# Kernel tuning notes

Hardware: AMD Instinct MI355X
Metric: run time of the kernel (lower is better)

## Reference

```python
import jax, jax.numpy as jnp
import numpy as np
import math

D_MODEL = 1024
NUM_HEADS = 16
BATCH = 4
SEQ = 2048

def setup_inputs() -> dict:
    key = jax.random.key(0)
    ks = jax.random.split(key, 7)
    s = 1.0 / math.sqrt(D_MODEL)
    return {
        "x": jax.random.normal(ks[0], (BATCH, SEQ, D_MODEL), dtype=jnp.float32),
        "Wq": jax.random.normal(ks[1], (D_MODEL, D_MODEL), dtype=jnp.float32) * s,
        "bq": jax.random.normal(ks[2], (D_MODEL,), dtype=jnp.float32) * s,
        "Wk": jax.random.normal(ks[3], (D_MODEL, D_MODEL), dtype=jnp.float32) * s,
        "bk": jax.random.normal(ks[4], (D_MODEL,), dtype=jnp.float32) * s,
        "Wv": jax.random.normal(ks[5], (D_MODEL, D_MODEL), dtype=jnp.float32) * s,
        "bv": jax.random.normal(ks[6], (D_MODEL,), dtype=jnp.float32) * s,
        "num_heads": NUM_HEADS,
    }

def reference(x, Wq, bq, Wk, bk, Wv, bv, num_heads):
    B, S, D = x.shape
    hd = D // num_heads
    scale = 1.0 / math.sqrt(D)  # NOTE: module scales by sqrt(d_model), not sqrt(head_dim)
    # torch nn.Linear: y = x @ W.T + b
    q = x @ Wq.T + bq
    k = x @ Wk.T + bk
    v = x @ Wv.T + bv
    # Faithful replication of the module's (non-standard) row-major view:
    # (B, S, D) -> (B*H, S, D/H)
    q = q.reshape(B * num_heads, -1, hd)
    k = k.reshape(B * num_heads, -1, hd)
    v = v.reshape(B * num_heads, -1, hd)
    scores = jnp.einsum('bqd,bkd->bqk', q, k) * scale  # [B*H, S, S]
    probs = jax.nn.softmax(scores, axis=-1)
    out = jnp.einsum('bqk,bkd->bqd', probs, v)
    return out.reshape(B, -1, D)
```

## Files before the change

kernel.cpp:

```cpp
#include <hip/hip_runtime.h>
#include <stdint.h>

typedef unsigned short u16;
typedef __attribute__((ext_vector_type(8))) short short8;
typedef __attribute__((ext_vector_type(4))) float f32x4;
typedef __attribute__((ext_vector_type(16))) float f32x16;
typedef __attribute__((ext_vector_type(2))) unsigned int uv2;
typedef __attribute__((ext_vector_type(4))) unsigned int uv4;

#define MFMA16(a, b, c) __builtin_amdgcn_mfma_f32_16x16x32_bf16((a), (b), (c), 0, 0, 0)
#define MFMA32(a, b, c) __builtin_amdgcn_mfma_f32_32x32x16_bf16((a), (b), (c), 0, 0, 0)
#define LOG2E 1.4426950408889634f
#define SCALE 0.03125f
#define KC (SCALE * LOG2E)

__device__ __forceinline__ u16 f2bf(float f) {
  union { float f; uint32_t u; } cv; cv.f = f;
  uint32_t u = cv.u;
  uint32_t r = (u + 0x7fffu + ((u >> 16) & 1u)) >> 16;
  return (u16)r;
}

__device__ __forceinline__ unsigned cvtpk(float lo, float hi) {
  unsigned r;
  asm("v_cvt_pk_bf16_f32 %0, %1, %2" : "=v"(r) : "v"(lo), "v"(hi));
  return r;
}

__device__ __forceinline__ void gld(const void* g, void* l) {
  __builtin_amdgcn_global_load_lds(
      (const __attribute__((address_space(1))) void*)g,
      (__attribute__((address_space(3))) void*)l, 16, 0, 0);
}

__device__ __forceinline__ const short8* tile8(const u16* base, int row, int c) {
  return (const short8*)(base + row * 64 + (((c) ^ (row & 7)) << 3));
}

__global__ void cvt4_kernel(const float* __restrict__ x, const float* __restrict__ wq,
                            const float* __restrict__ wk, const float* __restrict__ wv,
                            u16* __restrict__ xb, u16* __restrict__ wqb,
                            u16* __restrict__ wkb, u16* __restrict__ wvb) {
  const int NX8 = 1048576;
  const int NW8 = 131072;
  const int TOT = NX8 + 3 * NW8;
  int i = blockIdx.x * blockDim.x + threadIdx.x;
  const int stride = gridDim.x * blockDim.x;
  for (; i < TOT; i += stride) {
    const float* src; u16* dst; int j;
    if (i < NX8) { src = x; dst = xb; j = i; }
    else if (i < NX8 + NW8) { src = wq; dst = wqb; j = i - NX8; }
    else if (i < NX8 + 2 * NW8) { src = wk; dst = wkb; j = i - NX8 - NW8; }
    else { src = wv; dst = wvb; j = i - NX8 - 2 * NW8; }
    const f32x4* s = (const f32x4*)src + (size_t)j * 2;
    f32x4 a = s[0], b = s[1];
    short8 o;
    o[0] = (short)f2bf(a[0]); o[1] = (short)f2bf(a[1]);
    o[2] = (short)f2bf(a[2]); o[3] = (short)f2bf(a[3]);
    o[4] = (short)f2bf(b[0]); o[5] = (short)f2bf(b[1]);
    o[6] = (short)f2bf(b[2]); o[7] = (short)f2bf(b[3]);
    *((short8*)dst + j) = o;
  }
}

__global__ __launch_bounds__(256) void gemm_qkv(
    const u16* __restrict__ xb,
    const u16* __restrict__ wqb, const u16* __restrict__ wkb, const u16* __restrict__ wvb,
    const float* __restrict__ bq, const float* __restrict__ bk, const float* __restrict__ bv,
    u16* __restrict__ qo, u16* __restrict__ ko, u16* __restrict__ vo) {
  __shared__ __align__(16) u16 sm[2][128 * 64];

  const int bid = blockIdx.x;
  const int cx = bid & 7, qq = bid >> 3;
  const int m = ((qq & 7) << 3) + cx;
  const int nz = qq >> 3;
  const int n = nz / 3;
  const int z = nz - n * 3;
  const u16* W = (z == 0) ? wqb : (z == 1) ? wkb : wvb;
  const float* bias = (z == 0) ? bq : (z == 1) ? bk : bv;
  u16* out = (z == 0) ? qo : (z == 1) ? ko : vo;
  const float oscale = (z == 0) ? KC : 1.0f;
  const int m0 = m * 128, n0 = n * 128;

  const int t = threadIdx.x;
  const int lane = t & 63;
  const int w = t >> 6;
  const int l15 = lane & 15, l4 = lane >> 4;
  const int mw = (w >> 1) * 64, nw = (w & 1) * 64;

  const int srow8 = lane >> 3;
  const int ssw = ((lane & 7) ^ srow8) << 3;
  const u16* aG = xb + (size_t)(m0 + (w * 4) * 8 + srow8) * 1024 + ssw;
  const u16* bG = W + (size_t)(n0 + (w * 4) * 8 + srow8) * 1024 + ssw;
  u16* aL = &sm[0][0] + (w * 4) * 512 + lane * 8;
  u16* bL = &sm[1][0] + (w * 4) * 512 + lane * 8;

  float biasv[4];
#pragma unroll
  for (int nj = 0; nj < 4; nj++) biasv[nj] = bias[n0 + nw + nj * 16 + l15];

  const f32x4 fz = {0.f, 0.f, 0.f, 0.f};
  f32x4 acc[4][4];
#pragma unroll
  for (int i = 0; i < 4; i++)
#pragma unroll
    for (int j = 0; j < 4; j++) acc[i][j] = fz;

  for (int k0 = 0; k0 < 1024; k0 += 64) {
    __syncthreads();
#pragma unroll
    for (int cc = 0; cc < 4; cc++) {
      gld(aG + k0 + (size_t)cc * 8 * 1024, aL + cc * 512);
      gld(bG + k0 + (size_t)cc * 8 * 1024, bL + cc * 512);
    }
    __syncthreads();
#pragma unroll
    for (int kk = 0; kk < 2; kk++) {
      short8 af[4], bf[4];
#pragma unroll
      for (int mi = 0; mi < 4; mi++) af[mi] = *tile8(&sm[0][0], mw + mi * 16 + l15, kk * 4 + l4);
#pragma unroll
      for (int nj = 0; nj < 4; nj++) bf[nj] = *tile8(&sm[1][0], nw + nj * 16 + l15, kk * 4 + l4);
      __builtin_amdgcn_s_setprio(1);
#pragma unroll
      for (int mi = 0; mi < 4; mi++)
#pragma unroll
        for (int nj = 0; nj < 4; nj++)
          acc[mi][nj] = MFMA16(af[mi], bf[nj], acc[mi][nj]);
      __builtin_amdgcn_s_setprio(0);
    }
  }

  __syncthreads();
  u16* Cs = &sm[0][0] + w * 4096;
#pragma unroll
  for (int mi = 0; mi < 4; mi++)
#pragma unroll
    for (int nj = 0; nj < 4; nj++)
#pragma unroll
      for (int r = 0; r < 4; r++) {
        const int row = mi * 16 + l4 * 4 + r;
        const int col = nj * 16 + l15;
        Cs[row * 64 + (((col >> 3) ^ (row & 7)) << 3) + (col & 7)] =
            f2bf((acc[mi][nj][r] + biasv[nj]) * oscale);
      }
#pragma unroll
  for (int i = 0; i < 8; i++) {
    const int row = i * 8 + (lane >> 3);
    short8 vv = *tile8(Cs, row, lane & 7);
    *(short8*)(out + (size_t)(m0 + mw + row) * 1024 + n0 + nw + (lane & 7) * 8) = vv;
  }
}

__global__ void repack_v(const u16* __restrict__ v, u16* __restrict__ vpk) {
  __shared__ u16 L[4096];
  const int g = blockIdx.y, tt = blockIdx.x;
  const u16* src = v + (size_t)g * 131072 + (size_t)tt * 4096;
  const int t = threadIdx.x;
#pragma unroll
  for (int i = 0; i < 2; i++) {
    const int ccc = t + i * 256;
    const int r = ccc >> 3, d0 = (ccc & 7) * 8;
    short8 d = *(const short8*)(src + r * 64 + d0);
    const int c = r >> 3, j = r & 7;
    const int h2 = d0 >> 5;
    const int base = h2 * 2048 + (c >> 1) * 512 + (c & 1) * 256 + j;
#pragma unroll
    for (int jj = 0; jj < 8; jj++) L[base + ((d0 & 31) + jj) * 8] = (u16)d[jj];
  }
  __syncthreads();
  u16* dst = vpk + (size_t)((size_t)g * 32 + tt) * 4096;
#pragma unroll
  for (int i = 0; i < 2; i++) {
    const int ccc = t + i * 256;
    *(short8*)(dst + ccc * 8) = *(const short8*)(L + ccc * 8);
  }
}


__device__ __forceinline__ void qblock(f32x16& s, float& lsum, f32x16& o0, f32x16& o1,
                                       const short8* vf) {
  float p[16];
  float ps = 0.f;
#pragma unroll
  for (int i = 0; i < 16; i++) {
    p[i] = __builtin_amdgcn_exp2f(s[i]);
    ps += p[i];
  }
  lsum += ps;

  short8 pa0, pa1;
  {
    unsigned a0 = cvtpk(p[0], p[1]);
    unsigned a1 = cvtpk(p[2], p[3]);
    unsigned b0 = cvtpk(p[4], p[5]);
    unsigned b1 = cvtpk(p[6], p[7]);
    uv2 r0 = __builtin_amdgcn_permlane32_swap(a0, b0, false, false);
    uv2 r1 = __builtin_amdgcn_permlane32_swap(a1, b1, false, false);
    union { uv4 u; short8 s8; } cc;
    cc.u[0] = r0[0]; cc.u[1] = r1[0]; cc.u[2] = r0[1]; cc.u[3] = r1[1];
    pa0 = cc.s8;
  }
  {
    unsigned a0 = cvtpk(p[8], p[9]);
    unsigned a1 = cvtpk(p[10], p[11]);
    unsigned b0 = cvtpk(p[12], p[13]);
    unsigned b1 = cvtpk(p[14], p[15]);
    uv2 r0 = __builtin_amdgcn_permlane32_swap(a0, b0, false, false);
    uv2 r1 = __builtin_amdgcn_permlane32_swap(a1, b1, false, false);
    union { uv4 u; short8 s8; } cc;
    cc.u[0] = r0[0]; cc.u[1] = r1[0]; cc.u[2] = r0[1]; cc.u[3] = r1[1];
    pa1 = cc.s8;
  }
  __builtin_amdgcn_s_setprio(1);
  o0 = MFMA32(pa0, vf[0], o0);
  o0 = MFMA32(pa1, vf[1], o0);
  o1 = MFMA32(pa0, vf[2], o1);
  o1 = MFMA32(pa1, vf[3], o1);
  __builtin_amdgcn_s_setprio(0);
}

__global__ __launch_bounds__(256, 4) void attn_kernel(const u16* __restrict__ q,
                                                      const u16* __restrict__ k,
                                                      const u16* __restrict__ vpk,
                                                      float* __restrict__ out) {
  __shared__ __align__(16) u16 Ks[2][64 * 64];
  const int t = threadIdx.x, lane = t & 63, w = t >> 6;
  const int l31 = lane & 31, hi = lane >> 5;
  const int bid = blockIdx.x;
  const int cx = bid & 7, qq = bid >> 3;
  const int qt = qq & 15;
  const int g = ((qq >> 4) << 3) + cx;
  const size_t gb = (size_t)g * 131072;
  const int q0 = qt * 128 + w * 32;

  const u16* qp = q + gb + (size_t)(q0 + l31) * 64 + hi * 8;
  short8 qf[4];
#pragma unroll
  for (int ks = 0; ks < 4; ks++) qf[ks] = *(const short8*)(qp + ks * 16);

  const int srow8 = lane >> 3;
  const int ssw = ((lane & 7) ^ srow8) << 3;
  const u16* kG = k + gb + (size_t)((w * 2) * 8 + srow8) * 64 + ssw;
  const u16* vB = vpk + (size_t)g * 131072 + (size_t)lane * 8;

  f32x16 o0, o1;
#pragma unroll
  for (int i = 0; i < 16; i++) { o0[i] = 0.f; o1[i] = 0.f; }
  float lsum = 0.f;

  {
    u16* kD = &Ks[0][0] + (w * 2) * 512 + lane * 8;
#pragma unroll
    for (int cc = 0; cc < 2; cc++) gld(kG + (size_t)cc * 8 * 64, kD + cc * 512);
  }
  __syncthreads();

  int cur = 0;
  for (int tt = 0; tt < 32; ++tt) {
    if (tt < 31) {
      const int kvn = (tt + 1) * 64;
      u16* kD = &Ks[cur ^ 1][0] + (w * 2) * 512 + lane * 8;
#pragma unroll
      for (int cc = 0; cc < 2; cc++)
        gld(kG + (size_t)kvn * 64 + (size_t)cc * 8 * 64, kD + cc * 512);
    }
    const u16* Kb = &Ks[cur][0];
    const u16* vT = vB + (size_t)tt * 4096;
#pragma unroll
    for (int b = 0; b < 2; b++) {
      short8 vf[4];
#pragma unroll
      for (int h2 = 0; h2 < 2; h2++)
#pragma unroll
        for (int ksp = 0; ksp < 2; ksp++)
          vf[h2 * 2 + ksp] = *(const short8*)(vT + h2 * 2048 + ((b << 1) | ksp) * 512);
      f32x16 s;
#pragma unroll
      for (int i = 0; i < 16; i++) s[i] = 0.f;
      __builtin_amdgcn_s_setprio(1);
#pragma unroll
      for (int ks = 0; ks < 4; ks++) {
        short8 kf = *tile8(Kb, b * 32 + l31, (ks << 1) | hi);
        s = MFMA32(kf, qf[ks], s);
      }
      __builtin_amdgcn_s_setprio(0);
      qblock(s, lsum, o0, o1, vf);
    }
    __syncthreads();
    cur ^= 1;
  }

  float lt = lsum + __shfl_xor(lsum, 32);
  float inv = 1.0f / lt;
  float* ob = out + gb + (size_t)q0 * 64;
#pragma unroll
  for (int r = 0; r < 16; r++) {
    int qr = (r & 3) + 8 * (r >> 2) + 4 * hi;
    float ir = __shfl(inv, qr);
    ob[(size_t)qr * 64 + l31] = o0[r] * ir;
    ob[(size_t)qr * 64 + 32 + l31] = o1[r] * ir;
  }
}

extern "C" void kernel_launch(void* const* d_in, const int* in_sizes, int n_in,
                              void* d_out, int out_size, void* d_ws, size_t ws_size,
                              hipStream_t stream) {
  const float* x  = (const float*)d_in[0];
  const float* Wq = (const float*)d_in[1];
  const float* bq = (const float*)d_in[2];
  const float* Wk = (const float*)d_in[3];
  const float* bk = (const float*)d_in[4];
  const float* Wv = (const float*)d_in[5];
  const float* bv = (const float*)d_in[6];
  float* out = (float*)d_out;

  const size_t NX = 8388608;
  const size_t NW = 1048576;
  u16* ws = (u16*)d_ws;
  u16* xb  = ws;
  u16* wqb = xb + NX;
  u16* wkb = wqb + NW;
  u16* wvb = wkb + NW;
  u16* qb  = wvb + NW;
  u16* kb  = qb + NX;
  u16* vb  = kb + NX;
  u16* vpk = vb + NX;

  cvt4_kernel<<<2048, 256, 0, stream>>>(x, Wq, Wk, Wv, xb, wqb, wkb, wvb);

  gemm_qkv<<<1536, 256, 0, stream>>>(xb, wqb, wkb, wvb, bq, bk, bv, qb, kb, vb);

  repack_v<<<dim3(32, 64), 256, 0, stream>>>(vb, vpk);

  attn_kernel<<<1024, 256, 0, stream>>>(qb, kb, vpk, out);
}
```

Measured before the change: 154.9 us.

## Pre-pack K into MFMA fragment layout and load K directly from global

```diff
diff --git a/kernel.cpp b/kernel.cpp
--- a/kernel.cpp
+++ b/kernel.cpp
@@ -152,28 +152,34 @@
   }
 }
 
-__global__ void repack_v(const u16* __restrict__ v, u16* __restrict__ vpk) {
-  __shared__ u16 L[4096];
+__global__ void repack_kv(const u16* __restrict__ k, const u16* __restrict__ v,
+                          u16* __restrict__ kpk, u16* __restrict__ vpk) {
+  __shared__ __align__(16) u16 LK[4096];
+  __shared__ u16 LV[4096];
   const int g = blockIdx.y, tt = blockIdx.x;
-  const u16* src = v + (size_t)g * 131072 + (size_t)tt * 4096;
+  const size_t sb = (size_t)g * 131072 + (size_t)tt * 4096;
   const int t = threadIdx.x;
 #pragma unroll
   for (int i = 0; i < 2; i++) {
     const int ccc = t + i * 256;
     const int r = ccc >> 3, d0 = (ccc & 7) * 8;
-    short8 d = *(const short8*)(src + r * 64 + d0);
+    short8 dk = *(const short8*)(k + sb + (size_t)r * 64 + d0);
+    const int b = r >> 5, ks = d0 >> 4;
+    const int L = (r & 31) | (((d0 >> 3) & 1) << 5);
+    *(short8*)(LK + ((b * 4 + ks) << 9) + L * 8) = dk;
+    short8 dv = *(const short8*)(v + sb + (size_t)r * 64 + d0);
     const int c = r >> 3, j = r & 7;
     const int h2 = d0 >> 5;
     const int base = h2 * 2048 + (c >> 1) * 512 + (c & 1) * 256 + j;
 #pragma unroll
-    for (int jj = 0; jj < 8; jj++) L[base + ((d0 & 31) + jj) * 8] = (u16)d[jj];
+    for (int jj = 0; jj < 8; jj++) LV[base + ((d0 & 31) + jj) * 8] = (u16)dv[jj];
   }
   __syncthreads();
-  u16* dst = vpk + (size_t)((size_t)g * 32 + tt) * 4096;
 #pragma unroll
   for (int i = 0; i < 2; i++) {
     const int ccc = t + i * 256;
-    *(short8*)(dst + ccc * 8) = *(const short8*)(L + ccc * 8);
+    *(short8*)(kpk + sb + ccc * 8) = *(const short8*)(LK + ccc * 8);
+    *(short8*)(vpk + sb + ccc * 8) = *(const short8*)(LV + ccc * 8);
   }
 }
 
@@ -221,10 +227,9 @@
 }
 
 __global__ __launch_bounds__(256, 4) void attn_kernel(const u16* __restrict__ q,
-                                                      const u16* __restrict__ k,
+                                                      const u16* __restrict__ kpk,
                                                       const u16* __restrict__ vpk,
                                                       float* __restrict__ out) {
-  __shared__ __align__(16) u16 Ks[2][64 * 64];
   const int t = threadIdx.x, lane = t & 63, w = t >> 6;
   const int l31 = lane & 31, hi = lane >> 5;
   const int bid = blockIdx.x;
@@ -239,56 +244,56 @@
 #pragma unroll
   for (int ks = 0; ks < 4; ks++) qf[ks] = *(const short8*)(qp + ks * 16);
 
-  const int srow8 = lane >> 3;
-  const int ssw = ((lane & 7) ^ srow8) << 3;
-  const u16* kG = k + gb + (size_t)((w * 2) * 8 + srow8) * 64 + ssw;
-  const u16* vB = vpk + (size_t)g * 131072 + (size_t)lane * 8;
+  const u16* kP0 = kpk + gb + (size_t)lane * 8;
+  const u16* kP1 = kP0 + 2048;
+  const u16* vP0 = vpk + gb + (size_t)lane * 8;
+  const u16* vP1 = vP0 + 2048;
 
   f32x16 o0, o1;
 #pragma unroll
   for (int i = 0; i < 16; i++) { o0[i] = 0.f; o1[i] = 0.f; }
   float lsum = 0.f;
 
-  {
-    u16* kD = &Ks[0][0] + (w * 2) * 512 + lane * 8;
-#pragma unroll
-    for (int cc = 0; cc < 2; cc++) gld(kG + (size_t)cc * 8 * 64, kD + cc * 512);
-  }
-  __syncthreads();
-
-  int cur = 0;
   for (int tt = 0; tt < 32; ++tt) {
-    if (tt < 31) {
-      const int kvn = (tt + 1) * 64;
-      u16* kD = &Ks[cur ^ 1][0] + (w * 2) * 512 + lane * 8;
-#pragma unroll
-      for (int cc = 0; cc < 2; cc++)
-        gld(kG + (size_t)kvn * 64 + (size_t)cc * 8 * 64, kD + cc * 512);
-    }
-    const u16* Kb = &Ks[cur][0];
-    const u16* vT = vB + (size_t)tt * 4096;
-#pragma unroll
-    for (int b = 0; b < 2; b++) {
-      short8 vf[4];
-#pragma unroll
-      for (int h2 = 0; h2 < 2; h2++)
-#pragma unroll
-        for (int ksp = 0; ksp < 2; ksp++)
-          vf[h2 * 2 + ksp] = *(const short8*)(vT + h2 * 2048 + ((b << 1) | ksp) * 512);
+    {
+      short8 kf[4], vf[4];
+      kf[0] = *(const short8*)(kP0);
+      kf[1] = *(const short8*)(kP0 + 512);
+      kf[2] = *(const short8*)(kP0 + 1024);
+      kf[3] = *(const short8*)(kP0 + 1536);
+      vf[0] = *(const short8*)(vP0);
+      vf[1] = *(const short8*)(vP0 + 512);
+      vf[2] = *(const short8*)(vP1);
+      vf[3] = *(const short8*)(vP1 + 512);
       f32x16 s;
 #pragma unroll
       for (int i = 0; i < 16; i++) s[i] = 0.f;
       __builtin_amdgcn_s_setprio(1);
 #pragma unroll
-      for (int ks = 0; ks < 4; ks++) {
-        short8 kf = *tile8(Kb, b * 32 + l31, (ks << 1) | hi);
-        s = MFMA32(kf, qf[ks], s);
-      }
+      for (int ks = 0; ks < 4; ks++) s = MFMA32(kf[ks], qf[ks], s);
       __builtin_amdgcn_s_setprio(0);
       qblock(s, lsum, o0, o1, vf);
     }
-    __syncthreads();
-    cur ^= 1;
+    {
+      short8 kf[4], vf[4];
+      kf[0] = *(const short8*)(kP1);
+      kf[1] = *(const short8*)(kP1 + 512);
+      kf[2] = *(const short8*)(kP1 + 1024);
+      kf[3] = *(const short8*)(kP1 + 1536);
+      vf[0] = *(const short8*)(vP0 + 1024);
+      vf[1] = *(const short8*)(vP0 + 1536);
+      vf[2] = *(const short8*)(vP1 + 1024);
+      vf[3] = *(const short8*)(vP1 + 1536);
+      f32x16 s;
+#pragma unroll
+      for (int i = 0; i < 16; i++) s[i] = 0.f;
+      __builtin_amdgcn_s_setprio(1);
+#pragma unroll
+      for (int ks = 0; ks < 4; ks++) s = MFMA32(kf[ks], qf[ks], s);
+      __builtin_amdgcn_s_setprio(0);
+      qblock(s, lsum, o0, o1, vf);
+    }
+    kP0 += 4096; kP1 += 4096; vP0 += 4096; vP1 += 4096;
   }
 
   float lt = lsum + __shfl_xor(lsum, 32);
@@ -326,12 +331,13 @@
   u16* kb  = qb + NX;
   u16* vb  = kb + NX;
   u16* vpk = vb + NX;
+  u16* kpk = xb;
 
   cvt4_kernel<<<2048, 256, 0, stream>>>(x, Wq, Wk, Wv, xb, wqb, wkb, wvb);
 
   gemm_qkv<<<1536, 256, 0, stream>>>(xb, wqb, wkb, wvb, bq, bk, bv, qb, kb, vb);
 
-  repack_v<<<dim3(32, 64), 256, 0, stream>>>(vb, vpk);
-
-  attn_kernel<<<1024, 256, 0, stream>>>(qb, kb, vpk, out);
-}
+  repack_kv<<<dim3(32, 64), 256, 0, stream>>>(kb, vb, kpk, vpk);
+
+  attn_kernel<<<1024, 256, 0, stream>>>(qb, kpk, vpk, out);
+}
```

Result: slower. 170.1 us (+9.8%).
